# Kernel tuning notes

Measured on AMD Instinct MI355X. Metric: run time of the kernel, lower is better.

## Reference

```python
import jax, jax.numpy as jnp
import numpy as np

LEAKY = 0.2
BN_EPS = 1e-5
N_NODES = 50000
IN_F = 128
HID = 64
HEADS = 2
N_EDGES = 1600000


def _bn(x, gamma, beta):
    # BatchNorm1d in training mode: batch statistics over the node dim
    mu = jnp.mean(x, axis=0)
    var = jnp.mean((x - mu) ** 2, axis=0)
    return (x - mu) * jax.lax.rsqrt(var + BN_EPS) * gamma + beta


def _gat(x, src, dst, W, a_src, a_dst, bias, n):
    # W: [F_in, H*F], a_src/a_dst: [H, F]
    H, F = a_src.shape
    h = (x @ W).reshape(n, H, F)                      # [N,H,F]
    es = jnp.einsum('nhf,hf->nh', h, a_src)           # [N,H]
    ed = jnp.einsum('nhf,hf->nh', h, a_dst)           # [N,H]
    e = jax.nn.leaky_relu(es[src] + ed[dst], LEAKY)   # [E,H]
    m = jax.ops.segment_max(e, dst, num_segments=n)   # stable softmax per dst
    p = jnp.exp(e - m[dst])
    s = jax.ops.segment_sum(p, dst, num_segments=n)
    alpha = p / s[dst]                                # [E,H]
    out = jax.ops.segment_sum(h[src] * alpha[:, :, None], dst, num_segments=n)
    return out.reshape(n, H * F) + bias


def setup_inputs() -> dict:
    key = jax.random.key(0)
    ks = jax.random.split(key, 32)
    HF = HID * HEADS  # 128

    def g(k, shape, scale=0.1):
        return jax.random.normal(k, shape, dtype=jnp.float32) * scale

    inp = {
        'x': jax.random.normal(ks[0], (N_NODES, IN_F), dtype=jnp.float32),
        'edge_index': jax.random.randint(ks[1], (2, N_EDGES), 0, N_NODES, dtype=jnp.int64),
        # layer 1
        'W1': g(ks[2], (IN_F, HF)), 'as1': g(ks[3], (HEADS, HID)), 'ad1': g(ks[4], (HEADS, HID)),
        'gb1': jnp.zeros((HF,), jnp.float32),
        'lw1': g(ks[5], (IN_F, HF)), 'lb1': jnp.zeros((HF,), jnp.float32),
        'bg1': jnp.ones((IN_F,), jnp.float32), 'bb1': jnp.zeros((IN_F,), jnp.float32),
        # layer 2
        'W2': g(ks[6], (HF, HF)), 'as2': g(ks[7], (HEADS, HID)), 'ad2': g(ks[8], (HEADS, HID)),
        'gb2': jnp.zeros((HF,), jnp.float32),
        'lw2': g(ks[9], (HF, HF)), 'lb2': jnp.zeros((HF,), jnp.float32),
        'bg2': jnp.ones((HF,), jnp.float32), 'bb2': jnp.zeros((HF,), jnp.float32),
        # layer 3 (heads=1, out=2)
        'W3': g(ks[10], (HF, 2)), 'as3': g(ks[11], (1, 2)), 'ad3': g(ks[12], (1, 2)),
        'gb3': jnp.zeros((2,), jnp.float32),
        'lw3': g(ks[13], (HF, 2)), 'lb3': jnp.zeros((2,), jnp.float32),
        'bg3': jnp.ones((HF,), jnp.float32), 'bb3': jnp.zeros((HF,), jnp.float32),
    }
    return inp


def reference(x, edge_index,
              W1, as1, ad1, gb1, lw1, lb1, bg1, bb1,
              W2, as2, ad2, gb2, lw2, lb2, bg2, bb2,
              W3, as3, ad3, gb3, lw3, lb3, bg3, bb3):
    n = x.shape[0]
    loop = jnp.arange(n, dtype=edge_index.dtype)  # self-loops (PyG GAT default)
    src = jnp.concatenate([edge_index[0], loop])
    dst = jnp.concatenate([edge_index[1], loop])

    h = _bn(x, bg1, bb1)
    h = jax.nn.relu(h @ lw1 + lb1 + _gat(h, src, dst, W1, as1, ad1, gb1, n))
    h = _bn(h, bg2, bb2)
    h = jax.nn.relu(h @ lw2 + lb2 + _gat(h, src, dst, W2, as2, ad2, gb2, n))
    h = _bn(h, bg3, bb3)
    h = jax.nn.relu(h @ lw3 + lb3 + _gat(h, src, dst, W3, as3, ad3, gb3, n))
    return h
```

## Files before the change

### kernel.cpp

```cpp
#include <hip/hip_runtime.h>

#define LEAKY 0.2f
#define BN_EPS 1e-5f
#define BCHUNK 8192

typedef __bf16 v8bf __attribute__((ext_vector_type(8)));
typedef float v16f __attribute__((ext_vector_type(16)));
typedef float v2f __attribute__((ext_vector_type(2)));

__device__ __forceinline__ float wsum(float v) {
#pragma unroll
  for (int o = 32; o > 0; o >>= 1) v += __shfl_xor(v, o, 64);
  return v;
}

__device__ __forceinline__ float blo(unsigned u) { return __uint_as_float(u << 16); }
__device__ __forceinline__ float bhi(unsigned u) { return __uint_as_float(u & 0xffff0000u); }
__device__ __forceinline__ v2f bpair(unsigned u) {
  v2f r; r.x = __uint_as_float(u << 16); r.y = __uint_as_float(u & 0xffff0000u); return r;
}
__device__ __forceinline__ unsigned pack_bf16(float a, float b) {
  unsigned ua = __float_as_uint(a), ub = __float_as_uint(b);
  ua = (ua + 0x7fffu + ((ua >> 16) & 1u)) >> 16;
  ub = (ub + 0x7fffu + ((ub >> 16) & 1u)) >> 16;
  return ua | (ub << 16);
}
__device__ __forceinline__ unsigned short bf16of(float a) {
  unsigned ua = __float_as_uint(a);
  return (unsigned short)((ua + 0x7fffu + ((ua >> 16) & 1u)) >> 16);
}

__device__ __forceinline__ int edge_at(const void* ei, int is64, long long i) {
  return is64 ? (int)((const long long*)ei)[i] : ((const int*)ei)[i];
}


__device__ __forceinline__ void binA_body(int blk, const void* ei, int N, int E, int M,
                                          int nb, int nblk, int* counts, int* lds) {
  int* hist = lds;
  int* sflag = lds + 1024;
  int tid = threadIdx.x;
  if (tid < 64) {
    const long long* p = (const long long*)ei;
    long long v = p[tid];
    int bad = (v < 0 || v >= (long long)N) ? 1 : 0;
    unsigned long long mres = __ballot(bad);
    if (tid == 0) *sflag = (mres == 0ull) ? 1 : 0;
  }
  for (int j = tid; j < nb; j += 256) hist[j] = 0;
  __syncthreads();
  int is64 = *sflag;
  long long base = (long long)blk * BCHUNK;
  int cnt = (int)min((long long)BCHUNK, (long long)M - base);
  for (int i = tid; i < cnt; i += 256) {
    long long g = base + i;
    int d = (g < E) ? edge_at(ei, is64, (long long)E + g) : (int)(g - E);
    atomicAdd(&hist[d >> 7], 1);
  }
  __syncthreads();
  for (int j = tid; j < nb; j += 256) counts[(size_t)j * nblk + blk] = hist[j];
}

__device__ __forceinline__ void binC_body(int blk, const void* ei, int N, int E, int M,
                                          int nb, int nblk, const int* counts,
                                          unsigned* tmp, int* lds) {
  int* cur = lds;
  int* sflag = lds + 1024;
  int tid = threadIdx.x;
  if (tid < 64) {
    const long long* p = (const long long*)ei;
    long long v = p[tid];
    int bad = (v < 0 || v >= (long long)N) ? 1 : 0;
    unsigned long long mres = __ballot(bad);
    if (tid == 0) *sflag = (mres == 0ull) ? 1 : 0;
  }
  for (int j = tid; j < nb; j += 256) cur[j] = counts[(size_t)j * nblk + blk];
  __syncthreads();
  int is64 = *sflag;
  long long base = (long long)blk * BCHUNK;
  int cnt = (int)min((long long)BCHUNK, (long long)M - base);
  for (int i = tid; i < cnt; i += 256) {
    long long g = base + i;
    int s, d;
    if (g < E) { s = edge_at(ei, is64, g); d = edge_at(ei, is64, (long long)E + g); }
    else       { s = d = (int)(g - E); }
    int pos = atomicAdd(&cur[d >> 7], 1);
    tmp[pos] = ((unsigned)s << 7) | (unsigned)(d & 127);
  }
}

#define MM_SMEM (32 * 136 * 2 + 128 * 4 + 128 * 4)

__device__ __forceinline__ void mm_body(int blk, const void* xin, int packed,
    const float* stats, const float* gamma, const float* beta,
    const unsigned short* Bp, unsigned* hb, unsigned* linp,
    float* es, float* ed, int N, char* smem) {
  unsigned short* Al = (unsigned short*)smem;
  float* scl_s = (float*)(smem + 8704);
  float* sht_s = (float*)(smem + 8704 + 512);
  int tid = threadIdx.x;
  int lane = tid & 63;
  int w = tid >> 6;
  int rowBase = blk * 32;

  if (tid < 128) {
    float s = 0.f, s2 = 0.f;
#pragma unroll
    for (int r = 0; r < 8; ++r) {
      s += stats[r * 256 + tid];
      s2 += stats[r * 256 + 128 + tid];
    }
    float inv_n = 1.0f / (float)N;
    float mu = s * inv_n;
    float var = s2 * inv_n - mu * mu;
    float rs = rsqrtf(var + BN_EPS);
    float sc = gamma[tid] * rs;
    scl_s[tid] = sc;
    sht_s[tid] = beta[tid] - mu * sc;
  }

  v8bf bfrag[2][8];
#pragma unroll
  for (int t = 0; t < 2; ++t)
#pragma unroll
    for (int s = 0; s < 8; ++s) {
      int fi = ((2 * w + t) * 8 + s) * 64 + lane;
      bfrag[t][s] = *(const v8bf*)&Bp[(size_t)fi * 8];
    }
  __syncthreads();

  if (!packed) {
    const float* x = (const float*)xin;
    for (int q = tid; q < 32 * 32; q += 256) {
      int r = q >> 5, k4 = (q & 31) * 4;
      int row = rowBase + r;
      float4 v = make_float4(0.f, 0.f, 0.f, 0.f);
      if (row < N) v = *(const float4*)&x[(size_t)row * 128 + k4];
      unsigned p0 = pack_bf16(v.x * scl_s[k4] + sht_s[k4], v.y * scl_s[k4 + 1] + sht_s[k4 + 1]);
      unsigned p1 = pack_bf16(v.z * scl_s[k4 + 2] + sht_s[k4 + 2], v.w * scl_s[k4 + 3] + sht_s[k4 + 3]);
      *(uint2*)&Al[r * 136 + k4] = make_uint2(p0, p1);
    }
  } else {
    const unsigned* xp = (const unsigned*)xin;
    for (int q = tid; q < 32 * 16; q += 256) {
      int r = q >> 4, g = q & 15;
      int row = rowBase + r;
      uint4 u = make_uint4(0u, 0u, 0u, 0u);
      if (row < N) u = *(const uint4*)&xp[(size_t)row * 64 + g * 4];
      int f = g * 8;
      uint4 o;
      o.x = pack_bf16(blo(u.x) * scl_s[f] + sht_s[f], bhi(u.x) * scl_s[f + 1] + sht_s[f + 1]);
      o.y = pack_bf16(blo(u.y) * scl_s[f + 2] + sht_s[f + 2], bhi(u.y) * scl_s[f + 3] + sht_s[f + 3]);
      o.z = pack_bf16(blo(u.z) * scl_s[f + 4] + sht_s[f + 4], bhi(u.z) * scl_s[f + 5] + sht_s[f + 5]);
      o.w = pack_bf16(blo(u.w) * scl_s[f + 6] + sht_s[f + 6], bhi(u.w) * scl_s[f + 7] + sht_s[f + 7]);
      *(uint4*)&Al[r * 136 + f] = o;
    }
  }
  __syncthreads();

  int m = lane & 31, half = lane >> 5;
  v8bf afrag[8];
#pragma unroll
  for (int s = 0; s < 8; ++s)
    afrag[s] = *(const v8bf*)&Al[m * 136 + s * 16 + half * 8];

  v16f acc0 = {}, acc1 = {};
#pragma unroll
  for (int s = 0; s < 8; ++s) {
    acc0 = __builtin_amdgcn_mfma_f32_32x32x16_bf16(afrag[s], bfrag[0][s], acc0, 0, 0, 0);
    acc1 = __builtin_amdgcn_mfma_f32_32x32x16_bf16(afrag[s], bfrag[1][s], acc1, 0, 0, 0);
  }

  v16f acc2 = {};
  if (w == 0) {
#pragma unroll
    for (int s = 0; s < 8; ++s) {
      v8bf besf = *(const v8bf*)&Bp[(size_t)((64 + s) * 64 + lane) * 8];
      acc2 = __builtin_amdgcn_mfma_f32_32x32x16_bf16(afrag[s], besf, acc2, 0, 0, 0);
    }
  }

  int mlo = half * 4;
  int t0 = 2 * w, t1 = 2 * w + 1;
#pragma unroll
  for (int r = 0; r < 16; ++r) {
    int row = (r & 3) + 8 * (r >> 2) + mlo;
    int node = rowBase + row;
    float a0 = acc0[r], a1 = acc1[r];
    float b0 = __shfl_xor(a0, 1, 64);
    float b1 = __shfl_xor(a1, 1, 64);
    if (node < N && !(lane & 1)) {
      if (t0 < 4) {
        hb[(size_t)node * 64 + (t0 * 16 + (m >> 1))] = pack_bf16(a0, b0);
        hb[(size_t)node * 64 + (t1 * 16 + (m >> 1))] = pack_bf16(a1, b1);
      } else {
        linp[(size_t)node * 64 + ((t0 - 4) * 16 + (m >> 1))] = pack_bf16(a0, b0);
        linp[(size_t)node * 64 + ((t1 - 4) * 16 + (m >> 1))] = pack_bf16(a1, b1);
      }
    }
    if (w == 0 && m < 4 && node < N) {
      float v = acc2[r];
      if (m < 2) es[2 * node + (m & 1)] = v;
      else       ed[2 * node + (m & 1)] = v;
    }
  }
}


__global__ __launch_bounds__(256) void k_prepA(
    const float* __restrict__ W1, const float* __restrict__ LW1,
    const float* __restrict__ W2, const float* __restrict__ LW2,
    const float* __restrict__ as1, const float* __restrict__ ad1,
    const float* __restrict__ as2, const float* __restrict__ ad2,
    const float* __restrict__ x, int N,
    unsigned short* __restrict__ Bp1, unsigned short* __restrict__ Bp2,
    float* __restrict__ stats1,
    const void* ei, int E, int M, int nb, int nblk, int* counts) {
  __shared__ __align__(16) int lds[1025];
  int blk = blockIdx.x;
  int tid = threadIdx.x;
  if (blk >= 1058) { binA_body(blk - 1058, ei, N, E, M, nb, nblk, counts, lds); return; }
  if (blk >= 34) {
    int b = blk - 34;
    int f = tid & 127;
    int half = tid >> 7;
    float s = 0.f, s2 = 0.f;
    for (int r = b + half * 1024; r < N; r += 2048) {
      float v = x[(size_t)r * 128 + f];
      s += v; s2 += v * v;
    }
    float* rep = stats1 + (size_t)(b & 7) * 256;
    atomicAdd(&rep[f], s);
    atomicAdd(&rep[128 + f], s2);
    return;
  }
  if (blk >= 32) {
    float (*wes)[4] = (float(*)[4])lds;
    const float* W = (blk == 32) ? W1 : W2;
    const float* as_ = (blk == 32) ? as1 : as2;
    const float* ad_ = (blk == 32) ? ad1 : ad2;
    unsigned short* Bp = (blk == 32) ? Bp1 : Bp2;
#pragma unroll
    for (int it = 0; it < 2; ++it) {
      int k = tid & 127;
      int c = (tid >> 7) + 2 * it;
      const float* a = (c < 2) ? as_ : ad_;
      int hb2 = (c & 1) * 64;
      float sum = 0.f;
      for (int f = 0; f < 64; ++f) sum += W[k * 128 + hb2 + f] * a[hb2 + f];
      wes[k][c] = sum;
    }
    __syncthreads();
    for (int fr = tid; fr < 512; fr += 256) {
      int lane = fr & 63, s = fr >> 6;
      int n = lane & 31;
      int k0 = s * 16 + (lane >> 5) * 8;
      unsigned short tb[8];
#pragma unroll
      for (int j = 0; j < 8; ++j)
        tb[j] = bf16of((n < 4) ? wes[k0 + j][n] : 0.f);
      uint4 pk;
      pk.x = (unsigned)tb[0] | ((unsigned)tb[1] << 16);
      pk.y = (unsigned)tb[2] | ((unsigned)tb[3] << 16);
      pk.z = (unsigned)tb[4] | ((unsigned)tb[5] << 16);
      pk.w = (unsigned)tb[6] | ((unsigned)tb[7] << 16);
      int fi = (64 + s) * 64 + lane;
      *(uint4*)&Bp[(size_t)fi * 8] = pk;
    }
    return;
  }
  const float* W  = (blk < 16) ? W1 : W2;
  const float* LW = (blk < 16) ? LW1 : LW2;
  unsigned short* Bp = (blk < 16) ? Bp1 : Bp2;
  int fi = (blk & 15) * 256 + tid;
  int lane = fi & 63, s = (fi >> 6) & 7, t = fi >> 9;
  int n = t * 32 + (lane & 31);
  int k0 = s * 16 + (lane >> 5) * 8;
  unsigned short tb[8];
#pragma unroll
  for (int j = 0; j < 8; ++j) {
    int k = k0 + j;
    float v = (n < 128) ? W[k * 128 + n] : LW[k * 128 + (n - 128)];
    tb[j] = bf16of(v);
  }
  uint4 pk;
  pk.x = (unsigned)tb[0] | ((unsigned)tb[1] << 16);
  pk.y = (unsigned)tb[2] | ((unsigned)tb[3] << 16);
  pk.z = (unsigned)tb[4] | ((unsigned)tb[5] << 16);
  pk.w = (unsigned)tb[6] | ((unsigned)tb[7] << 16);
  *(uint4*)&Bp[(size_t)fi * 8] = pk;
}

__global__ __launch_bounds__(1024) void k_binScan(int* counts, int total_entries) {
  __shared__ int part[1024];
  int tid = threadIdx.x;
  int per = (total_entries + 1023) / 1024;
  int lo = tid * per;
  int hi = lo + per; if (hi > total_entries) hi = total_entries;
  int s = 0;
  int i = lo;
  for (; i + 8 <= hi; i += 8) {
    int c0 = counts[i], c1 = counts[i + 1], c2 = counts[i + 2], c3 = counts[i + 3];
    int c4 = counts[i + 4], c5 = counts[i + 5], c6 = counts[i + 6], c7 = counts[i + 7];
    s += ((c0 + c1) + (c2 + c3)) + ((c4 + c5) + (c6 + c7));
  }
  for (; i < hi; ++i) s += counts[i];
  part[tid] = s;
  __syncthreads();
  for (int off = 1; off < 1024; off <<= 1) {
    int add = (tid >= off) ? part[tid - off] : 0;
    __syncthreads();
    part[tid] += add;
    __syncthreads();
  }
  int run = (tid == 0) ? 0 : part[tid - 1];
  i = lo;
  for (; i + 8 <= hi; i += 8) {
    int c0 = counts[i], c1 = counts[i + 1], c2 = counts[i + 2], c3 = counts[i + 3];
    int c4 = counts[i + 4], c5 = counts[i + 5], c6 = counts[i + 6], c7 = counts[i + 7];
    counts[i] = run; run += c0;
    counts[i + 1] = run; run += c1;
    counts[i + 2] = run; run += c2;
    counts[i + 3] = run; run += c3;
    counts[i + 4] = run; run += c4;
    counts[i + 5] = run; run += c5;
    counts[i + 6] = run; run += c6;
    counts[i + 7] = run; run += c7;
  }
  for (; i < hi; ++i) {
    int c = counts[i];
    counts[i] = run;
    run += c;
  }
}

__global__ __launch_bounds__(256) void k_mmC(
    const void* __restrict__ xin, int packed,
    const float* __restrict__ stats, const float* __restrict__ gamma, const float* __restrict__ beta,
    const unsigned short* __restrict__ Bp,
    unsigned* __restrict__ hb, unsigned* __restrict__ linp,
    float* __restrict__ es, float* __restrict__ ed, int N, int gmm,
    const void* ei, int E, int M, int nb, int nblk, const int* counts, unsigned* tmp) {
  __shared__ __align__(16) char smem[MM_SMEM];
  int blk = blockIdx.x;
  if (blk < gmm) {
    mm_body(blk, xin, packed, stats, gamma, beta, Bp, hb, linp, es, ed, N, smem);
  } else {
    binC_body(blk - gmm, ei, N, E, M, nb, nblk, counts, tmp, (int*)smem);
  }
}

__global__ __launch_bounds__(256) void k_mm(
    const void* __restrict__ xin, int packed,
    const float* __restrict__ stats, const float* __restrict__ gamma, const float* __restrict__ beta,
    const unsigned short* __restrict__ Bp,
    unsigned* __restrict__ hb, unsigned* __restrict__ linp,
    float* __restrict__ es, float* __restrict__ ed, int N) {
  __shared__ __align__(16) char smem[MM_SMEM];
  mm_body(blockIdx.x, xin, packed, stats, gamma, beta, Bp, hb, linp, es, ed, N, smem);
}

__global__ __launch_bounds__(256) void k_binD(const unsigned* __restrict__ tmp,
                                              const int* __restrict__ counts,
                                              int nb, int nblk, int M, int N,
                                              int* __restrict__ rowptr, int* __restrict__ col) {
  __shared__ int scn[128];
  __shared__ int cur[128];
  int tid = threadIdx.x;
  int j = blockIdx.x;
  int base = counts[(size_t)j * nblk];
  int endv = (j + 1 < nb) ? counts[(size_t)(j + 1) * nblk] : M;
  int bc = endv - base;
  if (tid < 128) scn[tid] = 0;
  __syncthreads();
  for (int i = tid; i < bc; i += 256) atomicAdd(&scn[tmp[base + i] & 127], 1);
  __syncthreads();
  int v = (tid < 128) ? scn[tid] : 0;
  __syncthreads();
  for (int off = 1; off < 128; off <<= 1) {
    int add = (tid >= off && tid < 128) ? scn[tid - off] : 0;
    __syncthreads();
    if (tid < 128) scn[tid] += add;
    __syncthreads();
  }
  if (tid < 128) {
    int excl = scn[tid] - v;
    int d = (j << 7) + tid;
    if (d < N) rowptr[d] = base + excl;
    cur[tid] = base + excl;
  }
  __syncthreads();
  for (int i = tid; i < bc; i += 256) {
    unsigned w = tmp[base + i];
    int pos = atomicAdd(&cur[w & 127], 1);
    col[pos] = (int)(w >> 7);
  }
  if (j == nb - 1 && tid == 0) rowptr[N] = M;
}

__global__ __launch_bounds__(128) void k_bnstats(const unsigned* __restrict__ xp,
                                                 int N, float* sums) {
  int f = threadIdx.x;
  int q = f >> 1, hi = f & 1;
  float s = 0.f, s2 = 0.f;
  for (int r = blockIdx.x; r < N; r += gridDim.x) {
    unsigned u = xp[(size_t)r * 64 + q];
    float v = hi ? bhi(u) : blo(u);
    s += v; s2 += v * v;
  }
  float* rep = sums + (size_t)(blockIdx.x & 7) * 256;
  atomicAdd(&rep[f], s);
  atomicAdd(&rep[128 + f], s2);
}

__global__ __launch_bounds__(256) void k_agg(
    const int* __restrict__ rowptr, const int* __restrict__ col,
    const float* __restrict__ es, const float* __restrict__ ed,
    const unsigned* __restrict__ hb, const unsigned* __restrict__ linp,
    const float* __restrict__ lb, const float* __restrict__ gb,
    unsigned* __restrict__ xoutp, int N) {
  int lane = threadIdx.x & 63;
  int w = threadIdx.x >> 6;
  int d = blockIdx.x * 4 + w;
  if (d >= N) return;
  int start = rowptr[d], end = rowptr[d + 1];
  v2f edv = *(const v2f*)&ed[2 * d];
  int q = lane >> 4;
  int m = lane & 15;
  int head_hi = m >= 8;
  v2f zero = {0.f, 0.f};
  v2f lk = {LEAKY, LEAKY};

  v2f acc[4] = {zero, zero, zero, zero};
  v2f sp = zero;
  int i = start;
  for (; i + 16 <= end; i += 16) {
#pragma unroll
    for (int b = 0; b < 4; ++b) {
      int idx = i + 4 * b + q;
      int s = col[idx];
      v2f ev = *(const v2f*)&es[2 * s];
      uint4 u = *(const uint4*)&hb[(size_t)s * 64 + m * 4];
      v2f e = ev + edv;
      v2f le = __builtin_elementwise_max(e, zero) + lk * __builtin_elementwise_min(e, zero);
      v2f p; p.x = __expf(le.x); p.y = __expf(le.y);
      sp += p;
      float f = head_hi ? p.y : p.x;
      v2f fv = {f, f};
      acc[0] = __builtin_elementwise_fma(fv, bpair(u.x), acc[0]);
      acc[1] = __builtin_elementwise_fma(fv, bpair(u.y), acc[1]);
      acc[2] = __builtin_elementwise_fma(fv, bpair(u.z), acc[2]);
      acc[3] = __builtin_elementwise_fma(fv, bpair(u.w), acc[3]);
    }
  }
  for (; i < end; i += 4) {
    int idx = i + q;
    int valid = idx < end;
    int s = col[valid ? idx : end - 1];
    v2f ev = *(const v2f*)&es[2 * s];
    uint4 u = *(const uint4*)&hb[(size_t)s * 64 + m * 4];
    v2f e = ev + edv;
    v2f le = __builtin_elementwise_max(e, zero) + lk * __builtin_elementwise_min(e, zero);
    v2f p; p.x = __expf(le.x); p.y = __expf(le.y);
    if (!valid) p = zero;
    sp += p;
    float f = head_hi ? p.y : p.x;
    v2f fv = {f, f};
    acc[0] = __builtin_elementwise_fma(fv, bpair(u.x), acc[0]);
    acc[1] = __builtin_elementwise_fma(fv, bpair(u.y), acc[1]);
    acc[2] = __builtin_elementwise_fma(fv, bpair(u.z), acc[2]);
    acc[3] = __builtin_elementwise_fma(fv, bpair(u.w), acc[3]);
  }
#pragma unroll
  for (int k = 0; k < 4; ++k) {
    acc[k].x += __shfl_xor(acc[k].x, 16, 64);
    acc[k].x += __shfl_xor(acc[k].x, 32, 64);
    acc[k].y += __shfl_xor(acc[k].y, 16, 64);
    acc[k].y += __shfl_xor(acc[k].y, 32, 64);
  }
  sp.x += __shfl_xor(sp.x, 16, 64); sp.x += __shfl_xor(sp.x, 32, 64);
  sp.y += __shfl_xor(sp.y, 16, 64); sp.y += __shfl_xor(sp.y, 32, 64);

  if (q == 0) {
    float inv = 1.0f / (head_hi ? sp.y : sp.x);
    uint4 lv = *(const uint4*)&linp[(size_t)d * 64 + m * 4];
    int f8 = 8 * m;
    float4 lb0 = *(const float4*)&lb[f8], lb1 = *(const float4*)&lb[f8 + 4];
    float4 gb0 = *(const float4*)&gb[f8], gb1 = *(const float4*)&gb[f8 + 4];
    float v0 = blo(lv.x) + lb0.x + acc[0].x * inv + gb0.x;
    float v1 = bhi(lv.x) + lb0.y + acc[0].y * inv + gb0.y;
    float v2 = blo(lv.y) + lb0.z + acc[1].x * inv + gb0.z;
    float v3 = bhi(lv.y) + lb0.w + acc[1].y * inv + gb0.w;
    float v4 = blo(lv.z) + lb1.x + acc[2].x * inv + gb1.x;
    float v5 = bhi(lv.z) + lb1.y + acc[2].y * inv + gb1.y;
    float v6 = blo(lv.w) + lb1.z + acc[3].x * inv + gb1.z;
    float v7 = bhi(lv.w) + lb1.w + acc[3].y * inv + gb1.w;
    v0 = v0 > 0.f ? v0 : 0.f; v1 = v1 > 0.f ? v1 : 0.f;
    v2 = v2 > 0.f ? v2 : 0.f; v3 = v3 > 0.f ? v3 : 0.f;
    v4 = v4 > 0.f ? v4 : 0.f; v5 = v5 > 0.f ? v5 : 0.f;
    v6 = v6 > 0.f ? v6 : 0.f; v7 = v7 > 0.f ? v7 : 0.f;
    uint4 o;
    o.x = pack_bf16(v0, v1); o.y = pack_bf16(v2, v3);
    o.z = pack_bf16(v4, v5); o.w = pack_bf16(v6, v7);
    *(uint4*)&xoutp[(size_t)d * 64 + m * 4] = o;
  }
}

__global__ __launch_bounds__(256) void k_l3node(
    const unsigned* __restrict__ xp,
    const float* __restrict__ stats, const float* __restrict__ gamma, const float* __restrict__ beta,
    const float* __restrict__ W3, const float* __restrict__ LW3,
    const float* __restrict__ as3, const float* __restrict__ ad3,
    float* h3, float* lin3, float* es3, float* ed3, int N) {
  int lane = threadIdx.x & 63;
  int n = blockIdx.x * 4 + (threadIdx.x >> 6);
  if (n >= N) return;
  float inv_n = 1.0f / (float)N;
  int f0 = lane, f1 = 64 + lane;
  float su0 = 0.f, sq0 = 0.f, su1 = 0.f, sq1 = 0.f;
#pragma unroll
  for (int r = 0; r < 8; ++r) {
    su0 += stats[r * 256 + f0];  sq0 += stats[r * 256 + 128 + f0];
    su1 += stats[r * 256 + f1];  sq1 += stats[r * 256 + 128 + f1];
  }
  float mu0 = su0 * inv_n;
  float var0 = sq0 * inv_n - mu0 * mu0;
  float rs0 = rsqrtf(var0 + BN_EPS);
  float sc0 = gamma[f0] * rs0, sh0 = beta[f0] - mu0 * sc0;
  float mu1 = su1 * inv_n;
  float var1 = sq1 * inv_n - mu1 * mu1;
  float rs1 = rsqrtf(var1 + BN_EPS);
  float sc1 = gamma[f1] * rs1, sh1 = beta[f1] - mu1 * sc1;

  unsigned ua = xp[(size_t)n * 64 + (lane >> 1)];
  unsigned ub = xp[(size_t)n * 64 + 32 + (lane >> 1)];
  float xv0 = (lane & 1) ? bhi(ua) : blo(ua);
  float xv1 = (lane & 1) ? bhi(ub) : blo(ub);
  float xn0 = xv0 * sc0 + sh0;
  float xn1 = xv1 * sc1 + sh1;

  float2 w0 = *(const float2*)&W3[lane * 2];
  float2 w1 = *(const float2*)&W3[(64 + lane) * 2];
  float2 l0 = *(const float2*)&LW3[lane * 2];
  float2 l1 = *(const float2*)&LW3[(64 + lane) * 2];
  float hc0 = wsum(xn0 * w0.x + xn1 * w1.x);
  float hc1 = wsum(xn0 * w0.y + xn1 * w1.y);
  float lc0 = wsum(xn0 * l0.x + xn1 * l1.x);
  float lc1 = wsum(xn0 * l0.y + xn1 * l1.y);
  if (lane == 0) {
    h3[2 * n] = hc0; h3[2 * n + 1] = hc1;
    lin3[2 * n] = lc0; lin3[2 * n + 1] = lc1;
    es3[n] = hc0 * as3[0] + hc1 * as3[1];
    ed3[n] = hc0 * ad3[0] + hc1 * ad3[1];
  }
}

__global__ __launch_bounds__(256) void k_agg3(
    const int* __restrict__ rowptr, const int* __restrict__ col,
    const float* __restrict__ es, const float* __restrict__ ed,
    const float* __restrict__ h3, const float* __restrict__ lin3,
    const float* __restrict__ lb3, const float* __restrict__ gb3,
    float* __restrict__ out, int N) {
  int lane = threadIdx.x & 63;
  int d = blockIdx.x * 4 + (threadIdx.x >> 6);
  if (d >= N) return;
  int start = rowptr[d], end = rowptr[d + 1];
  float edd = ed[d];
  float ps = 0.f, a0 = 0.f, a1 = 0.f;
  for (int i = start + lane; i < end; i += 64) {
    int s = col[i];
    float e = es[s] + edd; e = e > 0.f ? e : LEAKY * e;
    float p = __expf(e);
    float2 hv = *(const float2*)&h3[2 * s];
    ps += p; a0 += p * hv.x; a1 += p * hv.y;
  }
  ps = wsum(ps); a0 = wsum(a0); a1 = wsum(a1);
  if (lane < 2) {
    float a = (lane == 0 ? a0 : a1) / ps;
    float v = lin3[2 * d + lane] + lb3[lane] + a + gb3[lane];
    out[2 * d + lane] = v > 0.f ? v : 0.f;
  }
}

extern "C" void kernel_launch(void* const* d_in, const int* in_sizes, int n_in,
                              void* d_out, int out_size, void* d_ws, size_t ws_size,
                              hipStream_t stream) {
  const float* x   = (const float*)d_in[0];
  const void*  ei  = d_in[1];
  const float* W1  = (const float*)d_in[2];
  const float* as1 = (const float*)d_in[3];
  const float* ad1 = (const float*)d_in[4];
  const float* gb1 = (const float*)d_in[5];
  const float* lw1 = (const float*)d_in[6];
  const float* lb1 = (const float*)d_in[7];
  const float* bg1 = (const float*)d_in[8];
  const float* bb1 = (const float*)d_in[9];
  const float* W2  = (const float*)d_in[10];
  const float* as2 = (const float*)d_in[11];
  const float* ad2 = (const float*)d_in[12];
  const float* gb2 = (const float*)d_in[13];
  const float* lw2 = (const float*)d_in[14];
  const float* lb2 = (const float*)d_in[15];
  const float* bg2 = (const float*)d_in[16];
  const float* bb2 = (const float*)d_in[17];
  const float* W3  = (const float*)d_in[18];
  const float* as3 = (const float*)d_in[19];
  const float* ad3 = (const float*)d_in[20];
  const float* gb3 = (const float*)d_in[21];
  const float* lw3 = (const float*)d_in[22];
  const float* lb3 = (const float*)d_in[23];
  const float* bg3 = (const float*)d_in[24];
  const float* bb3 = (const float*)d_in[25];
  float* out = (float*)d_out;

  int N = in_sizes[0] / 128;
  int E = in_sizes[1] / 2;
  int M = E + N;
  int nb = (N + 127) >> 7;
  int nblk = (M + BCHUNK - 1) / BCHUNK;

  char* wsp = (char*)d_ws;
  size_t off = 0;
  auto alloc = [&](size_t bytes) -> void* {
    void* p = wsp + off;
    off = (off + bytes + 255) & ~(size_t)255;
    return p;
  };
  int* rowptr   = (int*)alloc(((size_t)N + 1) * 4);
  int* col      = (int*)alloc((size_t)M * 4);
  unsigned* tmp = (unsigned*)alloc((size_t)M * 4);
  int* counts   = (int*)alloc(((size_t)nb * nblk + 1) * 4);
  float* st1    = (float*)alloc(8 * 256 * 4);
  float* st2    = (float*)alloc(8 * 256 * 4);
  float* st3    = (float*)alloc(8 * 256 * 4);
  unsigned short* Bp1 = (unsigned short*)alloc(4608 * 16);
  unsigned short* Bp2 = (unsigned short*)alloc(4608 * 16);
  unsigned* hbp  = (unsigned*)alloc((size_t)N * 64 * 4);
  unsigned* linp = (unsigned*)alloc((size_t)N * 64 * 4);
  unsigned* x2p  = (unsigned*)alloc((size_t)N * 64 * 4);
  float* es    = (float*)alloc((size_t)N * 2 * 4);
  float* edb   = (float*)alloc((size_t)N * 2 * 4);
  float* h3    = (float*)alloc((size_t)N * 2 * 4);
  float* lin3  = (float*)alloc((size_t)N * 2 * 4);
  float* es3   = (float*)alloc((size_t)N * 4);
  float* ed3   = (float*)alloc((size_t)N * 4);
  (void)ws_size; (void)n_in; (void)out_size;

  hipMemsetAsync(st1, 0, 3 * 8 * 256 * 4, stream);

  int gnode = (N + 3) / 4;
  int gmm = (N + 31) / 32;

  k_prepA<<<1058 + nblk, 256, 0, stream>>>(W1, lw1, W2, lw2, as1, ad1, as2, ad2,
                                           x, N, Bp1, Bp2, st1,
                                           ei, E, M, nb, nblk, counts);
  k_binScan<<<1, 1024, 0, stream>>>(counts, nb * nblk);
  k_mmC<<<gmm + nblk, 256, 0, stream>>>(x, 0, st1, bg1, bb1, Bp1, hbp, linp, es, edb, N,
                                        gmm, ei, E, M, nb, nblk, counts, tmp);
  k_binD<<<nb, 256, 0, stream>>>(tmp, counts, nb, nblk, M, N, rowptr, col);

  k_agg<<<gnode, 256, 0, stream>>>(rowptr, col, es, edb, hbp, linp, lb1, gb1, x2p, N);

  k_bnstats<<<1024, 128, 0, stream>>>(x2p, N, st2);
  k_mm<<<gmm, 256, 0, stream>>>(x2p, 1, st2, bg2, bb2, Bp2, hbp, linp, es, edb, N);
  k_agg<<<gnode, 256, 0, stream>>>(rowptr, col, es, edb, hbp, linp, lb2, gb2, x2p, N);

  k_bnstats<<<1024, 128, 0, stream>>>(x2p, N, st3);
  k_l3node<<<gnode, 256, 0, stream>>>(x2p, st3, bg3, bb3, W3, lw3, as3, ad3,
                                      h3, lin3, es3, ed3, N);
  k_agg3<<<gnode, 256, 0, stream>>>(rowptr, col, es3, ed3, h3, lin3, lb3, gb3, out, N);
}
```

Baseline: 433.6 us.

## Precompute per-node exponentials so edge softmax uses products instead of exp

Attention logits are now stored per node as exp(e) and exp(0.2*e), so each edge weight is a product of the source and destination factors. The leaky-relu branch is picked by comparing that product with 1, which removes per-edge transcendental work in the aggregation kernels. In exchange the per-node score gathers double in size. Skipping max-subtraction risks overflow for large logits. Block ordering in the fused launches is also swapped so the binning blocks are scheduled before the matmul and stats blocks.

```diff
diff --git a/kernel.cpp b/kernel.cpp
--- a/kernel.cpp
+++ b/kernel.cpp
@@ -94,7 +94,7 @@
 __device__ __forceinline__ void mm_body(int blk, const void* xin, int packed,
     const float* stats, const float* gamma, const float* beta,
     const unsigned short* Bp, unsigned* hb, unsigned* linp,
-    float* es, float* ed, int N, char* smem) {
+    float* esx, float* edx, int N, char* smem) {
   unsigned short* Al = (unsigned short*)smem;
   float* scl_s = (float*)(smem + 8704);
   float* sht_s = (float*)(smem + 8704 + 512);
@@ -200,8 +200,9 @@
     }
     if (w == 0 && m < 4 && node < N) {
       float v = acc2[r];
-      if (m < 2) es[2 * node + (m & 1)] = v;
-      else       ed[2 * node + (m & 1)] = v;
+      float pe = __expf(v), pq = __expf(LEAKY * v);
+      float* dst = (m < 2) ? esx : edx;
+      *(float2*)&dst[4 * (size_t)node + 2 * (m & 1)] = make_float2(pe, pq);
     }
   }
 }
@@ -219,7 +220,8 @@
   __shared__ __align__(16) int lds[1025];
   int blk = blockIdx.x;
   int tid = threadIdx.x;
-  if (blk >= 1058) { binA_body(blk - 1058, ei, N, E, M, nb, nblk, counts, lds); return; }
+  if (blk < nblk) { binA_body(blk, ei, N, E, M, nb, nblk, counts, lds); return; }
+  blk -= nblk;
   if (blk >= 34) {
     int b = blk - 34;
     int f = tid & 127;
@@ -339,14 +341,14 @@
     const float* __restrict__ stats, const float* __restrict__ gamma, const float* __restrict__ beta,
     const unsigned short* __restrict__ Bp,
     unsigned* __restrict__ hb, unsigned* __restrict__ linp,
-    float* __restrict__ es, float* __restrict__ ed, int N, int gmm,
+    float* __restrict__ esx, float* __restrict__ edx, int N,
     const void* ei, int E, int M, int nb, int nblk, const int* counts, unsigned* tmp) {
   __shared__ __align__(16) char smem[MM_SMEM];
   int blk = blockIdx.x;
-  if (blk < gmm) {
-    mm_body(blk, xin, packed, stats, gamma, beta, Bp, hb, linp, es, ed, N, smem);
+  if (blk < nblk) {
+    binC_body(blk, ei, N, E, M, nb, nblk, counts, tmp, (int*)smem);
   } else {
-    binC_body(blk - gmm, ei, N, E, M, nb, nblk, counts, tmp, (int*)smem);
+    mm_body(blk - nblk, xin, packed, stats, gamma, beta, Bp, hb, linp, esx, edx, N, smem);
   }
 }
 
@@ -355,9 +357,9 @@
     const float* __restrict__ stats, const float* __restrict__ gamma, const float* __restrict__ beta,
     const unsigned short* __restrict__ Bp,
     unsigned* __restrict__ hb, unsigned* __restrict__ linp,
-    float* __restrict__ es, float* __restrict__ ed, int N) {
+    float* __restrict__ esx, float* __restrict__ edx, int N) {
   __shared__ __align__(16) char smem[MM_SMEM];
-  mm_body(blockIdx.x, xin, packed, stats, gamma, beta, Bp, hb, linp, es, ed, N, smem);
+  mm_body(blockIdx.x, xin, packed, stats, gamma, beta, Bp, hb, linp, esx, edx, N, smem);
 }
 
 __global__ __launch_bounds__(256) void k_binD(const unsigned* __restrict__ tmp,
@@ -415,7 +417,7 @@
 
 __global__ __launch_bounds__(256) void k_agg(
     const int* __restrict__ rowptr, const int* __restrict__ col,
-    const float* __restrict__ es, const float* __restrict__ ed,
+    const float* __restrict__ esx, const float* __restrict__ edx,
     const unsigned* __restrict__ hb, const unsigned* __restrict__ linp,
     const float* __restrict__ lb, const float* __restrict__ gb,
     unsigned* __restrict__ xoutp, int N) {
@@ -424,28 +426,28 @@
   int d = blockIdx.x * 4 + w;
   if (d >= N) return;
   int start = rowptr[d], end = rowptr[d + 1];
-  v2f edv = *(const v2f*)&ed[2 * d];
+  float4 edv = *(const float4*)&edx[4 * (size_t)d];
   int q = lane >> 4;
   int m = lane & 15;
   int head_hi = m >= 8;
   v2f zero = {0.f, 0.f};
-  v2f lk = {LEAKY, LEAKY};
 
   v2f acc[4] = {zero, zero, zero, zero};
-  v2f sp = zero;
+  float s0 = 0.f, s1 = 0.f;
   int i = start;
   for (; i + 16 <= end; i += 16) {
 #pragma unroll
     for (int b = 0; b < 4; ++b) {
       int idx = i + 4 * b + q;
       int s = col[idx];
-      v2f ev = *(const v2f*)&es[2 * s];
+      float4 ev = *(const float4*)&esx[4 * (size_t)s];
       uint4 u = *(const uint4*)&hb[(size_t)s * 64 + m * 4];
-      v2f e = ev + edv;
-      v2f le = __builtin_elementwise_max(e, zero) + lk * __builtin_elementwise_min(e, zero);
-      v2f p; p.x = __expf(le.x); p.y = __expf(le.y);
-      sp += p;
-      float f = head_hi ? p.y : p.x;
+      float pe0 = ev.x * edv.x, q0 = ev.y * edv.y;
+      float pe1 = ev.z * edv.z, q1 = ev.w * edv.w;
+      float p0 = pe0 > 1.f ? pe0 : q0;
+      float p1 = pe1 > 1.f ? pe1 : q1;
+      s0 += p0; s1 += p1;
+      float f = head_hi ? p1 : p0;
       v2f fv = {f, f};
       acc[0] = __builtin_elementwise_fma(fv, bpair(u.x), acc[0]);
       acc[1] = __builtin_elementwise_fma(fv, bpair(u.y), acc[1]);
@@ -457,14 +459,15 @@
     int idx = i + q;
     int valid = idx < end;
     int s = col[valid ? idx : end - 1];
-    v2f ev = *(const v2f*)&es[2 * s];
+    float4 ev = *(const float4*)&esx[4 * (size_t)s];
     uint4 u = *(const uint4*)&hb[(size_t)s * 64 + m * 4];
-    v2f e = ev + edv;
-    v2f le = __builtin_elementwise_max(e, zero) + lk * __builtin_elementwise_min(e, zero);
-    v2f p; p.x = __expf(le.x); p.y = __expf(le.y);
-    if (!valid) p = zero;
-    sp += p;
-    float f = head_hi ? p.y : p.x;
+    float pe0 = ev.x * edv.x, q0 = ev.y * edv.y;
+    float pe1 = ev.z * edv.z, q1 = ev.w * edv.w;
+    float p0 = pe0 > 1.f ? pe0 : q0;
+    float p1 = pe1 > 1.f ? pe1 : q1;
+    if (!valid) { p0 = 0.f; p1 = 0.f; }
+    s0 += p0; s1 += p1;
+    float f = head_hi ? p1 : p0;
     v2f fv = {f, f};
     acc[0] = __builtin_elementwise_fma(fv, bpair(u.x), acc[0]);
     acc[1] = __builtin_elementwise_fma(fv, bpair(u.y), acc[1]);
@@ -478,11 +481,11 @@
     acc[k].y += __shfl_xor(acc[k].y, 16, 64);
     acc[k].y += __shfl_xor(acc[k].y, 32, 64);
   }
-  sp.x += __shfl_xor(sp.x, 16, 64); sp.x += __shfl_xor(sp.x, 32, 64);
-  sp.y += __shfl_xor(sp.y, 16, 64); sp.y += __shfl_xor(sp.y, 32, 64);
+  s0 += __shfl_xor(s0, 16, 64); s0 += __shfl_xor(s0, 32, 64);
+  s1 += __shfl_xor(s1, 16, 64); s1 += __shfl_xor(s1, 32, 64);
 
   if (q == 0) {
-    float inv = 1.0f / (head_hi ? sp.y : sp.x);
+    float inv = 1.0f / (head_hi ? s1 : s0);
     uint4 lv = *(const uint4*)&linp[(size_t)d * 64 + m * 4];
     int f8 = 8 * m;
     float4 lb0 = *(const float4*)&lb[f8], lb1 = *(const float4*)&lb[f8 + 4];
@@ -511,7 +514,7 @@
     const float* __restrict__ stats, const float* __restrict__ gamma, const float* __restrict__ beta,
     const float* __restrict__ W3, const float* __restrict__ LW3,
     const float* __restrict__ as3, const float* __restrict__ ad3,
-    float* h3, float* lin3, float* es3, float* ed3, int N) {
+    float* h3, float* lin3, float* es3x, float* ed3x, int N) {
   int lane = threadIdx.x & 63;
   int n = blockIdx.x * 4 + (threadIdx.x >> 6);
   if (n >= N) return;
@@ -550,14 +553,16 @@
   if (lane == 0) {
     h3[2 * n] = hc0; h3[2 * n + 1] = hc1;
     lin3[2 * n] = lc0; lin3[2 * n + 1] = lc1;
-    es3[n] = hc0 * as3[0] + hc1 * as3[1];
-    ed3[n] = hc0 * ad3[0] + hc1 * ad3[1];
+    float e = hc0 * as3[0] + hc1 * as3[1];
+    float dd = hc0 * ad3[0] + hc1 * ad3[1];
+    *(float2*)&es3x[2 * n] = make_float2(__expf(e), __expf(LEAKY * e));
+    *(float2*)&ed3x[2 * n] = make_float2(__expf(dd), __expf(LEAKY * dd));
   }
 }
 
 __global__ __launch_bounds__(256) void k_agg3(
     const int* __restrict__ rowptr, const int* __restrict__ col,
-    const float* __restrict__ es, const float* __restrict__ ed,
+    const float* __restrict__ es3x, const float* __restrict__ ed3x,
     const float* __restrict__ h3, const float* __restrict__ lin3,
     const float* __restrict__ lb3, const float* __restrict__ gb3,
     float* __restrict__ out, int N) {
@@ -565,12 +570,13 @@
   int d = blockIdx.x * 4 + (threadIdx.x >> 6);
   if (d >= N) return;
   int start = rowptr[d], end = rowptr[d + 1];
-  float edd = ed[d];
+  float2 edp = *(const float2*)&ed3x[2 * d];
   float ps = 0.f, a0 = 0.f, a1 = 0.f;
   for (int i = start + lane; i < end; i += 64) {
     int s = col[i];
-    float e = es[s] + edd; e = e > 0.f ? e : LEAKY * e;
-    float p = __expf(e);
+    float2 ep = *(const float2*)&es3x[2 * s];
+    float pe = ep.x * edp.x, pq = ep.y * edp.y;
+    float p = pe > 1.f ? pe : pq;
     float2 hv = *(const float2*)&h3[2 * s];
     ps += p; a0 += p * hv.x; a1 += p * hv.y;
   }
@@ -638,12 +644,12 @@
   unsigned* hbp  = (unsigned*)alloc((size_t)N * 64 * 4);
   unsigned* linp = (unsigned*)alloc((size_t)N * 64 * 4);
   unsigned* x2p  = (unsigned*)alloc((size_t)N * 64 * 4);
-  float* es    = (float*)alloc((size_t)N * 2 * 4);
-  float* edb   = (float*)alloc((size_t)N * 2 * 4);
+  float* esx   = (float*)alloc((size_t)N * 4 * 4);
+  float* edxb  = (float*)alloc((size_t)N * 4 * 4);
   float* h3    = (float*)alloc((size_t)N * 2 * 4);
   float* lin3  = (float*)alloc((size_t)N * 2 * 4);
-  float* es3   = (float*)alloc((size_t)N * 4);
-  float* ed3   = (float*)alloc((size_t)N * 4);
+  float* es3x  = (float*)alloc((size_t)N * 2 * 4);
+  float* ed3x  = (float*)alloc((size_t)N * 2 * 4);
   (void)ws_size; (void)n_in; (void)out_size;
 
   hipMemsetAsync(st1, 0, 3 * 8 * 256 * 4, stream);
@@ -651,22 +657,22 @@
   int gnode = (N + 3) / 4;
   int gmm = (N + 31) / 32;
 
-  k_prepA<<<1058 + nblk, 256, 0, stream>>>(W1, lw1, W2, lw2, as1, ad1, as2, ad2,
-                                           x, N, Bp1, Bp2, st1,
-                                           ei, E, M, nb, nblk, counts);
+  k_prepA<<<nblk + 34 + 1024, 256, 0, stream>>>(W1, lw1, W2, lw2, as1, ad1, as2, ad2,
+                                                x, N, Bp1, Bp2, st1,
+                                                ei, E, M, nb, nblk, counts);
   k_binScan<<<1, 1024, 0, stream>>>(counts, nb * nblk);
-  k_mmC<<<gmm + nblk, 256, 0, stream>>>(x, 0, st1, bg1, bb1, Bp1, hbp, linp, es, edb, N,
-                                        gmm, ei, E, M, nb, nblk, counts, tmp);
+  k_mmC<<<nblk + gmm, 256, 0, stream>>>(x, 0, st1, bg1, bb1, Bp1, hbp, linp, esx, edxb, N,
+                                        ei, E, M, nb, nblk, counts, tmp);
   k_binD<<<nb, 256, 0, stream>>>(tmp, counts, nb, nblk, M, N, rowptr, col);
 
-  k_agg<<<gnode, 256, 0, stream>>>(rowptr, col, es, edb, hbp, linp, lb1, gb1, x2p, N);
+  k_agg<<<gnode, 256, 0, stream>>>(rowptr, col, esx, edxb, hbp, linp, lb1, gb1, x2p, N);
 
   k_bnstats<<<1024, 128, 0, stream>>>(x2p, N, st2);
-  k_mm<<<gmm, 256, 0, stream>>>(x2p, 1, st2, bg2, bb2, Bp2, hbp, linp, es, edb, N);
-  k_agg<<<gnode, 256, 0, stream>>>(rowptr, col, es, edb, hbp, linp, lb2, gb2, x2p, N);
+  k_mm<<<gmm, 256, 0, stream>>>(x2p, 1, st2, bg2, bb2, Bp2, hbp, linp, esx, edxb, N);
+  k_agg<<<gnode, 256, 0, stream>>>(rowptr, col, esx, edxb, hbp, linp, lb2, gb2, x2p, N);
 
   k_bnstats<<<1024, 128, 0, stream>>>(x2p, N, st3);
   k_l3node<<<gnode, 256, 0, stream>>>(x2p, st3, bg3, bb3, W3, lw3, as3, ad3,
-                                      h3, lin3, es3, ed3, N);
-  k_agg3<<<gnode, 256, 0, stream>>>(rowptr, col, es3, ed3, h3, lin3, lb3, gb3, out, N);
-}
+                                      h3, lin3, es3x, ed3x, N);
+  k_agg3<<<gnode, 256, 0, stream>>>(rowptr, col, es3x, ed3x, h3, lin3, lb3, gb3, out, N);
+}
```

After: 443.1 us. +2.2%, slower.
